# Performance work log

Hardware: AMD Instinct MI355X
Metric: run time of the kernel (lower is better)

The kernel has to match this reference:

```python
import jax, jax.numpy as jnp
import numpy as np

B, D = 16384, 512
NUM_CLASSES, K = 90, 32


def _l2norm(v, axis=-1):
    return v / jnp.sqrt(jnp.sum(v * v, axis=axis, keepdims=True) + 1e-12)


def setup_inputs() -> dict:
    key = jax.random.key(0)
    k1, k2, k3 = jax.random.split(key, 3)
    x = jax.random.normal(k1, (B, D), dtype=jnp.float32)
    labels = jax.random.randint(k2, (B,), 0, NUM_CLASSES, dtype=jnp.int64)
    centers = jax.random.normal(k3, (NUM_CLASSES, K, D), dtype=jnp.float32)
    return {"x": x, "labels": labels, "centers": centers}


def reference(x, labels, centers):
    # l2Norm applied to centers at init and to x in forward
    xn = _l2norm(x, axis=1)                       # [B, D]
    cn = _l2norm(centers, axis=-1)                # [C, K, D]
    c = cn[labels]                                # gather: [B, K, D]
    # dst_k = 1 - <x_b, center_{label_b, k}>
    dst = 1.0 - jnp.einsum("bd,bkd->bk", xn, c)   # [B, K]
    score = jax.nn.softmax(2.0 - dst, axis=1)     # softmax over K sub-centers
    per_sample = jnp.sum(score * dst, axis=1)     # [B]
    return jnp.mean(per_sample)                   # scalar loss
```

## Files before the change

kernel.cpp:

```cpp
#include <hip/hip_runtime.h>
#include <hip/hip_bf16.h>

#define BB 16384
#define DD 512
#define NCLS 90
#define KC 32
#define BUCKET 512
#define NP 4

typedef __attribute__((ext_vector_type(8))) short short8;
typedef __attribute__((ext_vector_type(4))) float fx4;

static __device__ __forceinline__ short8 pack8s(float sc, float4 a, float4 b) {
    union { __hip_bfloat162 h[4]; short8 s; } u;
    u.h[0] = __float22bfloat162_rn(make_float2(a.x * sc, a.y * sc));
    u.h[1] = __float22bfloat162_rn(make_float2(a.z * sc, a.w * sc));
    u.h[2] = __float22bfloat162_rn(make_float2(b.x * sc, b.y * sc));
    u.h[3] = __float22bfloat162_rn(make_float2(b.z * sc, b.w * sc));
    return u.s;
}
static __device__ __forceinline__ short8 pack8(float4 a, float4 b) {
    union { __hip_bfloat162 h[4]; short8 s; } u;
    u.h[0] = __float22bfloat162_rn(make_float2(a.x, a.y));
    u.h[1] = __float22bfloat162_rn(make_float2(a.z, a.w));
    u.h[2] = __float22bfloat162_rn(make_float2(b.x, b.y));
    u.h[3] = __float22bfloat162_rn(make_float2(b.z, b.w));
    return u.s;
}

__global__ __launch_bounds__(1024)
void k_bin(const int* __restrict__ labels, int* __restrict__ idx, int* __restrict__ cnt) {
    __shared__ int lab[BB];
    __shared__ int wcnt[16];

    int t = threadIdx.x, w = t >> 6, lane = t & 63;
    int c = blockIdx.x;
    for (int j = t; j < BB / 4; j += 1024)
        ((int4*)lab)[j] = ((const int4*)labels)[j];
    __syncthreads();

    int seg4 = w * (BB / 4 / 16);
    int cw = 0;
#pragma unroll
    for (int jj = 0; jj < 4; jj++) {
        int4 v = ((int4*)lab)[seg4 + jj * 64 + lane];
        cw += (v.x == c) + (v.y == c) + (v.z == c) + (v.w == c);
    }
#pragma unroll
    for (int m = 1; m < 64; m <<= 1) cw += __shfl_xor(cw, m, 64);
    if (lane == 0) wcnt[w] = cw;
    __syncthreads();
    int pos = c * BUCKET;
    for (int ww = 0; ww < w; ww++) pos += wcnt[ww];
#pragma unroll
    for (int jj = 0; jj < 4; jj++) {
        int4 v = ((int4*)lab)[seg4 + jj * 64 + lane];
        int gbase = (seg4 + jj * 64 + lane) * 4;
        { bool m = (v.x == c); unsigned long long k = __ballot(m);
          if (m) idx[pos + __popcll(k & ((1ull << lane) - 1ull))] = gbase;     pos += __popcll(k); }
        { bool m = (v.y == c); unsigned long long k = __ballot(m);
          if (m) idx[pos + __popcll(k & ((1ull << lane) - 1ull))] = gbase + 1; pos += __popcll(k); }
        { bool m = (v.z == c); unsigned long long k = __ballot(m);
          if (m) idx[pos + __popcll(k & ((1ull << lane) - 1ull))] = gbase + 2; pos += __popcll(k); }
        { bool m = (v.w == c); unsigned long long k = __ballot(m);
          if (m) idx[pos + __popcll(k & ((1ull << lane) - 1ull))] = gbase + 3; pos += __popcll(k); }
    }
    if (t == 0) {
        int s = 0;
#pragma unroll
        for (int i = 0; i < 16; i++) s += wcnt[i];
        cnt[c] = s;
    }
}

__launch_bounds__(256, 2)
__global__ void k_main(const float* __restrict__ x,
                       const float* __restrict__ centers,
                       const int* __restrict__ cnt,
                       const int* __restrict__ idx,
                       float* __restrict__ partials) {
    __shared__ __align__(16) short c_lds[KC * DD];
    __shared__ __align__(16) short x_lds[32 * DD];
    __shared__ float S_lds[32][33];
    __shared__ float xinv[32];
    __shared__ float red4[4];

    int c = blockIdx.x >> 2;
    int p = blockIdx.x & 3;
    int n = cnt[c];
    int nch = (n + 31) >> 5;
    int t = threadIdx.x, w = t >> 6, lane = t & 63;
    float loss_acc = 0.f;

    if (p < nch) {
        int base = c * BUCKET;
        int row8 = t >> 3, l8 = t & 7;
        int mrow = ((w & 1) << 4) + (lane & 15);
        int nrow = ((w >> 1) << 4) + (lane & 15);

        float4 xva[8], xvb[8];
        {
            int off = p << 5;
            int rem = n - off;
            int r = (row8 < rem) ? row8 : (rem - 1);
            int g = idx[base + off + r];
            const float4* src = (const float4*)(x + (size_t)g * DD);
#pragma unroll
            for (int jj = 0; jj < 8; jj++) {
                xva[jj] = src[2 * l8 + 16 * jj];
                xvb[jj] = src[2 * l8 + 16 * jj + 1];
            }
        }

        {
            const float4* csrc = (const float4*)(centers + ((size_t)c * KC + row8) * DD);
            float4 cva[8], cvb[8];
#pragma unroll
            for (int jj = 0; jj < 8; jj++) {
                cva[jj] = csrc[2 * l8 + 16 * jj];
                cvb[jj] = csrc[2 * l8 + 16 * jj + 1];
            }
            float s = 0.f;
#pragma unroll
            for (int jj = 0; jj < 8; jj++) {
                float4 a = cva[jj], b4 = cvb[jj];
                s += a.x * a.x + a.y * a.y + a.z * a.z + a.w * a.w
                   + b4.x * b4.x + b4.y * b4.y + b4.z * b4.z + b4.w * b4.w;
            }
#pragma unroll
            for (int m = 1; m < 8; m <<= 1) s += __shfl_xor(s, m, 64);
            float sc = rsqrtf(s + 1e-12f);
#pragma unroll
            for (int jj = 0; jj < 8; jj++) {
                int c16 = l8 + 8 * jj;
                *(short8*)&c_lds[row8 * DD + ((c16 ^ (row8 & 7)) << 3)]
                    = pack8s(sc, cva[jj], cvb[jj]);
            }
        }

        for (int ch = p; ch < nch; ch += NP) {
            int off = ch << 5;
            int rem = n - off;

            {
                float nrm = 0.f;
#pragma unroll
                for (int jj = 0; jj < 8; jj++) {
                    int cc = l8 + 8 * jj;
                    float4 a = xva[jj], b4 = xvb[jj];
                    nrm += a.x * a.x + a.y * a.y + a.z * a.z + a.w * a.w
                         + b4.x * b4.x + b4.y * b4.y + b4.z * b4.z + b4.w * b4.w;
                    *(short8*)&x_lds[row8 * DD + ((cc ^ (row8 & 7)) << 3)] = pack8(a, b4);
                }
#pragma unroll
                for (int m = 1; m < 8; m <<= 1) nrm += __shfl_xor(nrm, m, 64);
                if (l8 == 0) xinv[row8] = rsqrtf(nrm + 1e-12f);
            }
            __syncthreads();

            fx4 acc = {0.f, 0.f, 0.f, 0.f};
#pragma unroll
            for (int ks = 0; ks < 16; ks++) {
                int c16a = ks * 4 + (lane >> 4);
                short8 av = *(const short8*)&x_lds[mrow * DD + ((c16a ^ (mrow & 7)) << 3)];
                short8 bv = *(const short8*)&c_lds[nrow * DD + ((c16a ^ (nrow & 7)) << 3)];
                acc = __builtin_amdgcn_mfma_f32_16x16x32_bf16(av, bv, acc, 0, 0, 0);
            }
#pragma unroll
            for (int j = 0; j < 4; j++) {
                int r = ((w & 1) << 4) + ((lane >> 4) << 2) + j;
                int col = ((w >> 1) << 4) + (lane & 15);
                S_lds[r][col] = acc[j];
            }

            if (ch + NP < nch) {
                int off2 = (ch + NP) << 5;
                int rem2 = n - off2;
                int r2 = (row8 < rem2) ? row8 : (rem2 - 1);
                int g2 = idx[base + off2 + r2];
                const float4* src2 = (const float4*)(x + (size_t)g2 * DD);
#pragma unroll
                for (int jj = 0; jj < 8; jj++) {
                    xva[jj] = src2[2 * l8 + 16 * jj];
                    xvb[jj] = src2[2 * l8 + 16 * jj + 1];
                }
            }
            __syncthreads();

            {
                float xv = xinv[row8];
                int q4 = l8 << 2;
                float s0 = S_lds[row8][q4 + 0] * xv;
                float s1 = S_lds[row8][q4 + 1] * xv;
                float s2 = S_lds[row8][q4 + 2] * xv;
                float s3 = S_lds[row8][q4 + 3] * xv;
                float e0 = __expf(s0), e1 = __expf(s1);
                float e2 = __expf(s2), e3 = __expf(s3);
                float Z = e0 + e1 + e2 + e3;
                float num = e0 * (1.f - s0) + e1 * (1.f - s1)
                          + e2 * (1.f - s2) + e3 * (1.f - s3);
#pragma unroll
                for (int m = 1; m < 8; m <<= 1) {
                    Z += __shfl_xor(Z, m, 64);
                    num += __shfl_xor(num, m, 64);
                }
                if (l8 == 0 && row8 < rem) loss_acc += num / Z;
            }
            __syncthreads();
        }
    }

#pragma unroll
    for (int m = 1; m < 64; m <<= 1) loss_acc += __shfl_xor(loss_acc, m, 64);
    if (lane == 0) red4[w] = loss_acc;
    __syncthreads();
    if (t == 0) partials[blockIdx.x] = red4[0] + red4[1] + red4[2] + red4[3];
}

__global__ void k_final(const float* __restrict__ partials, float* __restrict__ out) {
    __shared__ float red[256];
    int t = threadIdx.x;
    float s = 0.f;
    for (int i = t; i < NCLS * NP; i += 256) s += partials[i];
    red[t] = s;
    __syncthreads();
    for (int h = 128; h > 0; h >>= 1) {
        if (t < h) red[t] += red[t + h];
        __syncthreads();
    }
    if (t == 0) out[0] = red[0] * (1.0f / (float)BB);
}

extern "C" void kernel_launch(void* const* d_in, const int* in_sizes, int n_in,
                              void* d_out, int out_size, void* d_ws, size_t ws_size,
                              hipStream_t stream) {
    const float* x       = (const float*)d_in[0];
    const int*   labels  = (const int*)d_in[1];
    const float* centers = (const float*)d_in[2];
    float* out = (float*)d_out;

    char* ws = (char*)d_ws;
    int*   idx      = (int*)(ws + 0);
    int*   cnt      = (int*)(ws + 184320);
    float* partials = (float*)(ws + 196608);

    k_bin<<<NCLS, 1024, 0, stream>>>(labels, idx, cnt);
    k_main<<<NCLS * NP, 256, 0, stream>>>(x, centers, cnt, idx, partials);
    k_final<<<1, 256, 0, stream>>>(partials, out);
}
```

Before: 24.54 us.

## Fuse final reduction into main kernel via last-block atomic and halve per-class splits

Removes the separate final reduction kernel launch: each main block writes its partial, increments a global counter, and the last block sums all partials and writes the loss. The counter is reset in the binning kernel. The number of blocks per class drops from four to two, so each block processes more sample chunks. This saves launch overhead and extra blocks, at the cost of longer per-block serial work and reduced parallelism. It also drops the guard for empty chunks.

Result: slower. 28.65 us (+16.8%).

```diff
diff --git a/kernel.cpp b/kernel.cpp
--- a/kernel.cpp
+++ b/kernel.cpp
@@ -6,7 +6,7 @@
 #define NCLS 90
 #define KC 32
 #define BUCKET 512
-#define NP 4
+#define NP 2
 
 typedef __attribute__((ext_vector_type(8))) short short8;
 typedef __attribute__((ext_vector_type(4))) float fx4;
@@ -29,12 +29,14 @@
 }
 
 __global__ __launch_bounds__(1024)
-void k_bin(const int* __restrict__ labels, int* __restrict__ idx, int* __restrict__ cnt) {
+void k_bin(const int* __restrict__ labels, int* __restrict__ idx, int* __restrict__ cnt,
+           int* __restrict__ counter) {
     __shared__ int lab[BB];
     __shared__ int wcnt[16];
 
     int t = threadIdx.x, w = t >> 6, lane = t & 63;
     int c = blockIdx.x;
+    if (c == 0 && t == 0) *counter = 0;
     for (int j = t; j < BB / 4; j += 1024)
         ((int4*)lab)[j] = ((const int4*)labels)[j];
     __syncthreads();
@@ -78,21 +80,24 @@
                        const float* __restrict__ centers,
                        const int* __restrict__ cnt,
                        const int* __restrict__ idx,
-                       float* __restrict__ partials) {
+                       float* __restrict__ partials,
+                       int* __restrict__ counter,
+                       float* __restrict__ out) {
     __shared__ __align__(16) short c_lds[KC * DD];
     __shared__ __align__(16) short x_lds[32 * DD];
     __shared__ float S_lds[32][33];
     __shared__ float xinv[32];
     __shared__ float red4[4];
-
-    int c = blockIdx.x >> 2;
-    int p = blockIdx.x & 3;
+    __shared__ int lastflag;
+
+    int c = blockIdx.x >> 1;
+    int p = blockIdx.x & 1;
     int n = cnt[c];
     int nch = (n + 31) >> 5;
     int t = threadIdx.x, w = t >> 6, lane = t & 63;
     float loss_acc = 0.f;
 
-    if (p < nch) {
+    {
         int base = c * BUCKET;
         int row8 = t >> 3, l8 = t & 7;
         int mrow = ((w & 1) << 4) + (lane & 15);
@@ -214,21 +219,24 @@
     for (int m = 1; m < 64; m <<= 1) loss_acc += __shfl_xor(loss_acc, m, 64);
     if (lane == 0) red4[w] = loss_acc;
     __syncthreads();
-    if (t == 0) partials[blockIdx.x] = red4[0] + red4[1] + red4[2] + red4[3];
-}
-
-__global__ void k_final(const float* __restrict__ partials, float* __restrict__ out) {
-    __shared__ float red[256];
-    int t = threadIdx.x;
-    float s = 0.f;
-    for (int i = t; i < NCLS * NP; i += 256) s += partials[i];
-    red[t] = s;
-    __syncthreads();
-    for (int h = 128; h > 0; h >>= 1) {
-        if (t < h) red[t] += red[t + h];
+    if (t == 0) {
+        partials[blockIdx.x] = red4[0] + red4[1] + red4[2] + red4[3];
+        __threadfence();
+        int old = atomicAdd(counter, 1);
+        lastflag = (old == (int)gridDim.x - 1);
+    }
+    __syncthreads();
+    if (lastflag) {
+        __threadfence();
+        float s = 0.f;
+        for (int i = t; i < NCLS * NP; i += 256)
+            s += __hip_atomic_load(&partials[i], __ATOMIC_RELAXED, __HIP_MEMORY_SCOPE_AGENT);
+#pragma unroll
+        for (int m = 1; m < 64; m <<= 1) s += __shfl_xor(s, m, 64);
+        if (lane == 0) red4[w] = s;
         __syncthreads();
-    }
-    if (t == 0) out[0] = red[0] * (1.0f / (float)BB);
+        if (t == 0) out[0] = (red4[0] + red4[1] + red4[2] + red4[3]) * (1.0f / (float)BB);
+    }
 }
 
 extern "C" void kernel_launch(void* const* d_in, const int* in_sizes, int n_in,
@@ -242,9 +250,9 @@
     char* ws = (char*)d_ws;
     int*   idx      = (int*)(ws + 0);
     int*   cnt      = (int*)(ws + 184320);
+    int*   counter  = (int*)(ws + 184832);
     float* partials = (float*)(ws + 196608);
 
-    k_bin<<<NCLS, 1024, 0, stream>>>(labels, idx, cnt);
-    k_main<<<NCLS * NP, 256, 0, stream>>>(x, centers, cnt, idx, partials);
-    k_final<<<1, 256, 0, stream>>>(partials, out);
-}
+    k_bin<<<NCLS, 1024, 0, stream>>>(labels, idx, cnt, counter);
+    k_main<<<NCLS * NP, 256, 0, stream>>>(x, centers, cnt, idx, partials, counter, out);
+}
```

## Precompute normalized bf16 centers in binning kernel, load via direct global-to-LDS

Applied to the files above, without the earlier changes.

Center normalization and bf16 packing move from k_main, where each of the four blocks per class redid them, into k_bin, which writes a bf16 copy of the centers to the workspace. k_main then fills its swizzled LDS tile with global_load_lds DMA instead of loading fp32 into registers and converting. This removes redundant normalization work and halves the center bytes k_main reads. In exchange it adds a workspace round trip and puts the center-load latency inside k_bin, and the direct LDS load depends on its swizzle addressing and on waitcnt handling before the LDS is read.

Measured after the change: 24.95 us. About the same (+1.7%).

```diff
diff --git a/kernel.cpp b/kernel.cpp
--- a/kernel.cpp
+++ b/kernel.cpp
@@ -27,16 +27,41 @@
     u.h[3] = __float22bfloat162_rn(make_float2(b.z, b.w));
     return u.s;
 }
+static __device__ __forceinline__ void gload_lds16(const void* g, void* l) {
+    __builtin_amdgcn_global_load_lds(
+        (const __attribute__((address_space(1))) void*)g,
+        (__attribute__((address_space(3))) void*)l, 16, 0, 0);
+}
 
 __global__ __launch_bounds__(1024)
-void k_bin(const int* __restrict__ labels, int* __restrict__ idx, int* __restrict__ cnt) {
+void k_bin(const int* __restrict__ labels, const float* __restrict__ centers,
+           short* __restrict__ cni, int* __restrict__ idx, int* __restrict__ cnt) {
     __shared__ int lab[BB];
     __shared__ int wcnt[16];
 
     int t = threadIdx.x, w = t >> 6, lane = t & 63;
     int c = blockIdx.x;
+
+    int r = t >> 5, s = t & 31;
+    const float4* csrc = (const float4*)(centers + ((size_t)c * KC + r) * DD);
+    float4 cv0 = csrc[4 * s + 0], cv1 = csrc[4 * s + 1];
+    float4 cv2 = csrc[4 * s + 2], cv3 = csrc[4 * s + 3];
+
     for (int j = t; j < BB / 4; j += 1024)
         ((int4*)lab)[j] = ((const int4*)labels)[j];
+
+    {
+        float nr = cv0.x * cv0.x + cv0.y * cv0.y + cv0.z * cv0.z + cv0.w * cv0.w
+                 + cv1.x * cv1.x + cv1.y * cv1.y + cv1.z * cv1.z + cv1.w * cv1.w
+                 + cv2.x * cv2.x + cv2.y * cv2.y + cv2.z * cv2.z + cv2.w * cv2.w
+                 + cv3.x * cv3.x + cv3.y * cv3.y + cv3.z * cv3.z + cv3.w * cv3.w;
+#pragma unroll
+        for (int m = 1; m < 32; m <<= 1) nr += __shfl_xor(nr, m, 64);
+        float sc = rsqrtf(nr + 1e-12f);
+        short* dst = cni + ((size_t)c * KC + r) * DD + s * 16;
+        *(short8*)(dst)     = pack8s(sc, cv0, cv1);
+        *(short8*)(dst + 8) = pack8s(sc, cv2, cv3);
+    }
     __syncthreads();
 
     int seg4 = w * (BB / 4 / 16);
@@ -66,16 +91,16 @@
           if (m) idx[pos + __popcll(k & ((1ull << lane) - 1ull))] = gbase + 3; pos += __popcll(k); }
     }
     if (t == 0) {
-        int s = 0;
-#pragma unroll
-        for (int i = 0; i < 16; i++) s += wcnt[i];
-        cnt[c] = s;
+        int ssum = 0;
+#pragma unroll
+        for (int i = 0; i < 16; i++) ssum += wcnt[i];
+        cnt[c] = ssum;
     }
 }
 
 __launch_bounds__(256, 2)
 __global__ void k_main(const float* __restrict__ x,
-                       const float* __restrict__ centers,
+                       const short* __restrict__ cni,
                        const int* __restrict__ cnt,
                        const int* __restrict__ idx,
                        float* __restrict__ partials) {
@@ -98,6 +123,13 @@
         int mrow = ((w & 1) << 4) + (lane & 15);
         int nrow = ((w >> 1) << 4) + (lane & 15);
 
+        const short* cbase = cni + (size_t)c * KC * DD;
+#pragma unroll
+        for (int it = 0; it < 8; it++) {
+            int q = t + 256 * it;
+            int drow = q >> 6, cc = q & 63;
+            gload_lds16(cbase + drow * DD + (cc ^ (drow & 7)) * 8, &c_lds[q * 8]);
+        }
         float4 xva[8], xvb[8];
         {
             int off = p << 5;
@@ -109,32 +141,6 @@
             for (int jj = 0; jj < 8; jj++) {
                 xva[jj] = src[2 * l8 + 16 * jj];
                 xvb[jj] = src[2 * l8 + 16 * jj + 1];
-            }
-        }
-
-        {
-            const float4* csrc = (const float4*)(centers + ((size_t)c * KC + row8) * DD);
-            float4 cva[8], cvb[8];
-#pragma unroll
-            for (int jj = 0; jj < 8; jj++) {
-                cva[jj] = csrc[2 * l8 + 16 * jj];
-                cvb[jj] = csrc[2 * l8 + 16 * jj + 1];
-            }
-            float s = 0.f;
-#pragma unroll
-            for (int jj = 0; jj < 8; jj++) {
-                float4 a = cva[jj], b4 = cvb[jj];
-                s += a.x * a.x + a.y * a.y + a.z * a.z + a.w * a.w
-                   + b4.x * b4.x + b4.y * b4.y + b4.z * b4.z + b4.w * b4.w;
-            }
-#pragma unroll
-            for (int m = 1; m < 8; m <<= 1) s += __shfl_xor(s, m, 64);
-            float sc = rsqrtf(s + 1e-12f);
-#pragma unroll
-            for (int jj = 0; jj < 8; jj++) {
-                int c16 = l8 + 8 * jj;
-                *(short8*)&c_lds[row8 * DD + ((c16 ^ (row8 & 7)) << 3)]
-                    = pack8s(sc, cva[jj], cvb[jj]);
             }
         }
 
@@ -240,11 +246,12 @@
     float* out = (float*)d_out;
 
     char* ws = (char*)d_ws;
-    int*   idx      = (int*)(ws + 0);
-    int*   cnt      = (int*)(ws + 184320);
-    float* partials = (float*)(ws + 196608);
-
-    k_bin<<<NCLS, 1024, 0, stream>>>(labels, idx, cnt);
-    k_main<<<NCLS * NP, 256, 0, stream>>>(x, centers, cnt, idx, partials);
+    short* cni      = (short*)(ws + 0);
+    int*   idx      = (int*)(ws + 3145728);
+    int*   cnt      = (int*)(ws + 3407872);
+    float* partials = (float*)(ws + 3473408);
+
+    k_bin<<<NCLS, 1024, 0, stream>>>(labels, centers, cni, idx, cnt);
+    k_main<<<NCLS * NP, 256, 0, stream>>>(x, cni, cnt, idx, partials);
     k_final<<<1, 256, 0, stream>>>(partials, out);
 }
```

## Fuse label binning into main kernel using per-block LDS index list

Applied to the files above, without the earlier changes.

Removes the separate binning kernel. Each main block now scans all labels itself, counts matches for its class and compacts the matching row indices into shared memory. The centers load is moved ahead of the scan so its latency overlaps with the label pass. This saves one kernel launch and the global idx/cnt round trip. In exchange each of the 360 blocks rereads the 64KB label array, so the scan work is repeated four times per class, and the bucket is assumed to hold at most 512 samples.

Result: no change. 24.88 us (+1.4%).

```diff
diff --git a/kernel.cpp b/kernel.cpp
--- a/kernel.cpp
+++ b/kernel.cpp
@@ -5,7 +5,6 @@
 #define DD 512
 #define NCLS 90
 #define KC 32
-#define BUCKET 512
 #define NP 4
 
 typedef __attribute__((ext_vector_type(8))) short short8;
@@ -28,73 +27,69 @@
     return u.s;
 }
 
-__global__ __launch_bounds__(1024)
-void k_bin(const int* __restrict__ labels, int* __restrict__ idx, int* __restrict__ cnt) {
-    __shared__ int lab[BB];
-    __shared__ int wcnt[16];
-
-    int t = threadIdx.x, w = t >> 6, lane = t & 63;
-    int c = blockIdx.x;
-    for (int j = t; j < BB / 4; j += 1024)
-        ((int4*)lab)[j] = ((const int4*)labels)[j];
-    __syncthreads();
-
-    int seg4 = w * (BB / 4 / 16);
-    int cw = 0;
-#pragma unroll
-    for (int jj = 0; jj < 4; jj++) {
-        int4 v = ((int4*)lab)[seg4 + jj * 64 + lane];
-        cw += (v.x == c) + (v.y == c) + (v.z == c) + (v.w == c);
-    }
-#pragma unroll
-    for (int m = 1; m < 64; m <<= 1) cw += __shfl_xor(cw, m, 64);
-    if (lane == 0) wcnt[w] = cw;
-    __syncthreads();
-    int pos = c * BUCKET;
-    for (int ww = 0; ww < w; ww++) pos += wcnt[ww];
-#pragma unroll
-    for (int jj = 0; jj < 4; jj++) {
-        int4 v = ((int4*)lab)[seg4 + jj * 64 + lane];
-        int gbase = (seg4 + jj * 64 + lane) * 4;
-        { bool m = (v.x == c); unsigned long long k = __ballot(m);
-          if (m) idx[pos + __popcll(k & ((1ull << lane) - 1ull))] = gbase;     pos += __popcll(k); }
-        { bool m = (v.y == c); unsigned long long k = __ballot(m);
-          if (m) idx[pos + __popcll(k & ((1ull << lane) - 1ull))] = gbase + 1; pos += __popcll(k); }
-        { bool m = (v.z == c); unsigned long long k = __ballot(m);
-          if (m) idx[pos + __popcll(k & ((1ull << lane) - 1ull))] = gbase + 2; pos += __popcll(k); }
-        { bool m = (v.w == c); unsigned long long k = __ballot(m);
-          if (m) idx[pos + __popcll(k & ((1ull << lane) - 1ull))] = gbase + 3; pos += __popcll(k); }
-    }
-    if (t == 0) {
-        int s = 0;
-#pragma unroll
-        for (int i = 0; i < 16; i++) s += wcnt[i];
-        cnt[c] = s;
-    }
-}
-
 __launch_bounds__(256, 2)
 __global__ void k_main(const float* __restrict__ x,
                        const float* __restrict__ centers,
-                       const int* __restrict__ cnt,
-                       const int* __restrict__ idx,
+                       const int* __restrict__ labels,
                        float* __restrict__ partials) {
     __shared__ __align__(16) short c_lds[KC * DD];
     __shared__ __align__(16) short x_lds[32 * DD];
     __shared__ float S_lds[32][33];
     __shared__ float xinv[32];
     __shared__ float red4[4];
+    __shared__ int idx_lds[512];
+    __shared__ int wcnt[4];
 
     int c = blockIdx.x >> 2;
     int p = blockIdx.x & 3;
-    int n = cnt[c];
+    int t = threadIdx.x, w = t >> 6, lane = t & 63;
+    int row8 = t >> 3, l8 = t & 7;
+
+    const float4* csrc = (const float4*)(centers + ((size_t)c * KC + row8) * DD);
+    float4 cva[8], cvb[8];
+#pragma unroll
+    for (int jj = 0; jj < 8; jj++) {
+        cva[jj] = csrc[2 * l8 + 16 * jj];
+        cvb[jj] = csrc[2 * l8 + 16 * jj + 1];
+    }
+
+    int seg4 = w * (BB / 4 / 4);
+    {
+        int cw = 0;
+#pragma unroll
+        for (int jj = 0; jj < 16; jj++) {
+            int4 v = ((const int4*)labels)[seg4 + jj * 64 + lane];
+            cw += (v.x == c) + (v.y == c) + (v.z == c) + (v.w == c);
+        }
+#pragma unroll
+        for (int m = 1; m < 64; m <<= 1) cw += __shfl_xor(cw, m, 64);
+        if (lane == 0) wcnt[w] = cw;
+    }
+    __syncthreads();
+    int n = wcnt[0] + wcnt[1] + wcnt[2] + wcnt[3];
+    {
+        int pos = 0;
+        for (int ww = 0; ww < w; ww++) pos += wcnt[ww];
+#pragma unroll
+        for (int jj = 0; jj < 16; jj++) {
+            int4 v = ((const int4*)labels)[seg4 + jj * 64 + lane];
+            int gbase = (seg4 + jj * 64 + lane) * 4;
+            { bool m = (v.x == c); unsigned long long k = __ballot(m);
+              if (m) idx_lds[pos + __popcll(k & ((1ull << lane) - 1ull))] = gbase;     pos += __popcll(k); }
+            { bool m = (v.y == c); unsigned long long k = __ballot(m);
+              if (m) idx_lds[pos + __popcll(k & ((1ull << lane) - 1ull))] = gbase + 1; pos += __popcll(k); }
+            { bool m = (v.z == c); unsigned long long k = __ballot(m);
+              if (m) idx_lds[pos + __popcll(k & ((1ull << lane) - 1ull))] = gbase + 2; pos += __popcll(k); }
+            { bool m = (v.w == c); unsigned long long k = __ballot(m);
+              if (m) idx_lds[pos + __popcll(k & ((1ull << lane) - 1ull))] = gbase + 3; pos += __popcll(k); }
+        }
+    }
+    __syncthreads();
+
     int nch = (n + 31) >> 5;
-    int t = threadIdx.x, w = t >> 6, lane = t & 63;
     float loss_acc = 0.f;
 
     if (p < nch) {
-        int base = c * BUCKET;
-        int row8 = t >> 3, l8 = t & 7;
         int mrow = ((w & 1) << 4) + (lane & 15);
         int nrow = ((w >> 1) << 4) + (lane & 15);
 
@@ -103,7 +98,7 @@
             int off = p << 5;
             int rem = n - off;
             int r = (row8 < rem) ? row8 : (rem - 1);
-            int g = idx[base + off + r];
+            int g = idx_lds[off + r];
             const float4* src = (const float4*)(x + (size_t)g * DD);
 #pragma unroll
             for (int jj = 0; jj < 8; jj++) {
@@ -113,13 +108,6 @@
         }
 
         {
-            const float4* csrc = (const float4*)(centers + ((size_t)c * KC + row8) * DD);
-            float4 cva[8], cvb[8];
-#pragma unroll
-            for (int jj = 0; jj < 8; jj++) {
-                cva[jj] = csrc[2 * l8 + 16 * jj];
-                cvb[jj] = csrc[2 * l8 + 16 * jj + 1];
-            }
             float s = 0.f;
 #pragma unroll
             for (int jj = 0; jj < 8; jj++) {
@@ -177,7 +165,7 @@
                 int off2 = (ch + NP) << 5;
                 int rem2 = n - off2;
                 int r2 = (row8 < rem2) ? row8 : (rem2 - 1);
-                int g2 = idx[base + off2 + r2];
+                int g2 = idx_lds[off2 + r2];
                 const float4* src2 = (const float4*)(x + (size_t)g2 * DD);
 #pragma unroll
                 for (int jj = 0; jj < 8; jj++) {
@@ -239,12 +227,8 @@
     const float* centers = (const float*)d_in[2];
     float* out = (float*)d_out;
 
-    char* ws = (char*)d_ws;
-    int*   idx      = (int*)(ws + 0);
-    int*   cnt      = (int*)(ws + 184320);
-    float* partials = (float*)(ws + 196608);
-
-    k_bin<<<NCLS, 1024, 0, stream>>>(labels, idx, cnt);
-    k_main<<<NCLS * NP, 256, 0, stream>>>(x, centers, cnt, idx, partials);
+    float* partials = (float*)d_ws;
+
+    k_main<<<NCLS * NP, 256, 0, stream>>>(x, centers, labels, partials);
     k_final<<<1, 256, 0, stream>>>(partials, out);
 }
```
